# Kernel optimization log

Hardware: AMD Instinct MI355X
Metric: run time of the kernel (lower is better)

The kernel has to match this reference:

```python
import jax, jax.numpy as jnp
import numpy as np

NUM_HEADS = 8
DIM_HEAD = 64
GROUPS = 32
EPS = 1e-5


def setup_inputs() -> dict:
    key = jax.random.key(0)
    k1, k2, k3 = jax.random.split(key, 3)
    C = 512
    inner = NUM_HEADS * DIM_HEAD  # 512
    x = jax.random.normal(k1, (8, C, 32, 32), dtype=jnp.float32)
    gamma = jnp.ones((C,), dtype=jnp.float32)
    beta = jnp.zeros((C,), dtype=jnp.float32)
    w_qkv = jax.random.normal(k2, (3 * inner, C), dtype=jnp.float32) * 0.02
    w_out = jax.random.normal(k3, (C, inner), dtype=jnp.float32) * 0.02
    return {"x": x, "gamma": gamma, "beta": beta, "w_qkv": w_qkv, "w_out": w_out}


def group_norm(x, gamma, beta):
    b, c, h, w = x.shape
    xg = x.reshape(b, GROUPS, c // GROUPS, h, w)
    mean = jnp.mean(xg, axis=(2, 3, 4), keepdims=True)
    var = jnp.var(xg, axis=(2, 3, 4), keepdims=True)
    xn = ((xg - mean) * jax.lax.rsqrt(var + EPS)).reshape(b, c, h, w)
    return xn * gamma[None, :, None, None] + beta[None, :, None, None]


def reference(x, gamma, beta, w_qkv, w_out):
    b, c, h, w = x.shape
    H, d = NUM_HEADS, DIM_HEAD
    inner = H * d
    scale = d ** (-0.5)
    residual = x
    xn = group_norm(x, gamma, beta)
    # 1x1 conv (no bias) == channel matmul
    qkv = jnp.einsum('bchw,oc->bohw', xn, w_qkv)  # [b, 3*inner, h, w]
    q, k, v = jnp.split(qkv, 3, axis=1)
    def to_heads(t):
        # b (H d) h w -> b H (h w) d
        return t.reshape(b, H, d, h * w).transpose(0, 1, 3, 2)
    q, k, v = to_heads(q), to_heads(k), to_heads(v)
    attn = jnp.einsum('bhid,bhjd->bhij', q, k) * scale  # [b,H,hw,hw]
    attn = jax.nn.softmax(attn, axis=-1)
    out = jnp.einsum('bhij,bhjd->bhid', attn, v)  # [b,H,hw,d]
    # b H (h w) d -> b (H d) h w
    out = out.transpose(0, 1, 3, 2).reshape(b, inner, h, w)
    out = jnp.einsum('bchw,oc->bohw', out, w_out)
    return out + residual
```

## Files before the change

kernel.cpp:

```cpp
#include <hip/hip_runtime.h>


typedef __attribute__((ext_vector_type(8))) short bf16x8;
typedef __attribute__((ext_vector_type(4))) short bf16x4;
typedef __attribute__((ext_vector_type(4))) float f32x4;
typedef __attribute__((ext_vector_type(16))) float f32x16;

#define NB 8
#define NC 512
#define HW 1024
#define NHEAD 8
#define DHEAD 64
#define GROUPS 32
#define CPG 16
#define QKV_N 1536

#define GLL16(gaddr, ldsaddr)                                                  \
    __builtin_amdgcn_global_load_lds(                                          \
        (const __attribute__((address_space(1))) unsigned*)(gaddr),            \
        (__attribute__((address_space(3))) unsigned*)(ldsaddr), 16, 0, 0)

__device__ alignas(64) short g_xn[(size_t)8192 * 512];
__device__ alignas(64) short g_qkv[(size_t)8192 * 1536];
__device__ alignas(64) short g_vt[(size_t)64 * 64 * 1024];
__device__ alignas(64) short g_attno[(size_t)8192 * 512];
__device__ alignas(64) short g_wqkv[(size_t)1536 * 512];
__device__ alignas(64) short g_wout[(size_t)512 * 512];

__device__ __forceinline__ float b2f(short h) {
    union { unsigned u; float f; } v;
    v.u = ((unsigned)(unsigned short)h) << 16;
    return v.f;
}
__device__ __forceinline__ short f2b(float f) {
    union { float f; unsigned u; } v;
    v.f = f;
    unsigned r = v.u + 0x7fff + ((v.u >> 16) & 1);
    return (short)(r >> 16);
}

__global__ __launch_bounds__(256) void prep_kernel(
    const float* __restrict__ x, const float* __restrict__ gamma,
    const float* __restrict__ beta, const float* __restrict__ wqkv,
    const float* __restrict__ wout) {
    int tid = threadIdx.x;
    if (blockIdx.x >= 256) {
        int wb = blockIdx.x - 256;
        for (int i = wb * 256 + tid; i < 1536 * 512; i += 64 * 256) {
            float v = wqkv[i];
            if (i < 512 * 512) v *= 0.18033688011112042f;
            g_wqkv[i] = f2b(v);
        }
        for (int i = wb * 256 + tid; i < 512 * 512; i += 64 * 256)
            g_wout[i] = f2b(wout[i]);
        return;
    }
    int b = blockIdx.x >> 5, g = blockIdx.x & 31;
    __shared__ alignas(16) short tile[CPG][HW];
    __shared__ float red[2][4];
    __shared__ float sg[CPG], sb[CPG];
    if (tid < CPG) {
        int cg = g * CPG + tid;
        sg[tid] = gamma[cg];
        sb[tid] = beta[cg];
    }
    const float* xb = x + (size_t)b * NC * HW + (size_t)g * CPG * HW;
    float s1 = 0.f, s2 = 0.f;
    #pragma unroll
    for (int it = 0; it < 8; it++) {
        int idx = tid + it * 256;
        f32x4 v0 = *(const f32x4*)(xb + idx * 8);
        f32x4 v1 = *(const f32x4*)(xb + idx * 8 + 4);
        bf16x8 w;
        #pragma unroll
        for (int j = 0; j < 4; j++) {
            s1 += v0[j] + v1[j]; s2 += v0[j] * v0[j] + v1[j] * v1[j];
            w[j] = f2b(v0[j]); w[j + 4] = f2b(v1[j]);
        }
        *(bf16x8*)(&((short*)tile)[idx * 8]) = w;
    }
    #pragma unroll
    for (int off = 32; off; off >>= 1) { s1 += __shfl_xor(s1, off); s2 += __shfl_xor(s2, off); }
    int wid = tid >> 6;
    if ((tid & 63) == 0) { red[0][wid] = s1; red[1][wid] = s2; }
    __syncthreads();
    float t1 = red[0][0] + red[0][1] + red[0][2] + red[0][3];
    float t2 = red[1][0] + red[1][1] + red[1][2] + red[1][3];
    float mean = t1 * (1.f / 16384.f);
    float var  = t2 * (1.f / 16384.f) - mean * mean;
    float inv  = rsqrtf(var + 1e-5f);
    #pragma unroll
    for (int p = 0; p < 4; p++) {
        int s = tid * 4 + p;
        bf16x8 pk0, pk1;
        #pragma unroll
        for (int cc = 0; cc < 8; cc++) {
            pk0[cc] = f2b((b2f(tile[cc][s])     - mean) * inv * sg[cc]     + sb[cc]);
            pk1[cc] = f2b((b2f(tile[cc + 8][s]) - mean) * inv * sg[cc + 8] + sb[cc + 8]);
        }
        size_t dst = ((size_t)(b * HW + s)) * NC + g * CPG;
        *(bf16x8*)(g_xn + dst)     = pk0;
        *(bf16x8*)(g_xn + dst + 8) = pk1;
    }
}

__global__ __launch_bounds__(256) void gemm_qkv() {
    const int K = NC;
    int tid = threadIdx.x, lane = tid & 63, wid = tid >> 6;
    int quad = lane >> 4, l15 = lane & 15;
    int row0 = blockIdx.x * 128;
    int col0 = blockIdx.y * 128;
    __shared__ alignas(16) short sa[128 * 64];
    __shared__ alignas(16) short sbuf[128 * 64];
    int r_lo = lane >> 3;
    int s_log = (lane & 7) ^ r_lo;
    int swz = l15 & 7;
    const short* ga = g_xn   + (size_t)(row0 + wid * 32 + r_lo) * K + s_log * 8;
    const short* gb = g_wqkv + (size_t)(col0 + wid * 32 + r_lo) * K + s_log * 8;
    int mw = (wid >> 1) * 64, nw = (wid & 1) * 64;
    f32x4 acc[4][4] = {};
    for (int k = 0; k < K; k += 64) {
        #pragma unroll
        for (int c = 0; c < 4; c++) {
            GLL16(ga + (size_t)(c * 8) * K + k, &sa[(wid * 32 + c * 8) * 64]);
            GLL16(gb + (size_t)(c * 8) * K + k, &sbuf[(wid * 32 + c * 8) * 64]);
        }
        __syncthreads();
        bf16x8 af0[4], af1[4], bf0[4], bf1[4];
        #pragma unroll
        for (int m = 0; m < 4; m++) {
            int row = mw + m * 16 + l15;
            af0[m] = *(const bf16x8*)&sa[row * 64 + ((quad ^ swz) * 8)];
            af1[m] = *(const bf16x8*)&sa[row * 64 + (((4 + quad) ^ swz) * 8)];
        }
        #pragma unroll
        for (int n = 0; n < 4; n++) {
            int row = nw + n * 16 + l15;
            bf0[n] = *(const bf16x8*)&sbuf[row * 64 + ((quad ^ swz) * 8)];
            bf1[n] = *(const bf16x8*)&sbuf[row * 64 + (((4 + quad) ^ swz) * 8)];
        }
        #pragma unroll
        for (int m = 0; m < 4; m++)
            #pragma unroll
            for (int n = 0; n < 4; n++) {
                acc[m][n] = __builtin_amdgcn_mfma_f32_16x16x32_bf16(af0[m], bf0[n], acc[m][n], 0, 0, 0);
                acc[m][n] = __builtin_amdgcn_mfma_f32_16x16x32_bf16(af1[m], bf1[n], acc[m][n], 0, 0, 0);
            }
        __syncthreads();
    }
    #pragma unroll
    for (int m = 0; m < 4; m++)
        #pragma unroll
        for (int n = 0; n < 4; n++)
            #pragma unroll
            for (int r = 0; r < 4; r++) {
                int row = row0 + mw + m * 16 + quad * 4 + r;
                int col = col0 + nw + n * 16 + l15;
                g_qkv[(size_t)row * QKV_N + col] = f2b(acc[m][n][r]);
            }
}

__global__ __launch_bounds__(256) void transpose_v() {
    int bh = blockIdx.x & 63, st = blockIdx.x >> 6;
    int b = bh >> 3, h = bh & 7;
    int tid = threadIdx.x;
    __shared__ alignas(16) short tile[64][72];
    int s0 = st * 64;
    #pragma unroll
    for (int cc = 0; cc < 2; cc++) {
        int idx = tid + cc * 256;
        int s = idx >> 3, dc = idx & 7;
        *(bf16x8*)&tile[s][dc * 8] =
            *(const bf16x8*)(g_qkv + ((size_t)(b * HW + s0 + s)) * QKV_N + 1024 + h * DHEAD + dc * 8);
    }
    __syncthreads();
    #pragma unroll
    for (int cc = 0; cc < 2; cc++) {
        int idx = tid + cc * 256;
        int d = idx & 63, sc = idx >> 6;
        bf16x8 o;
        #pragma unroll
        for (int j = 0; j < 8; j++) o[j] = tile[sc * 8 + j][d];
        *(bf16x8*)(g_vt + ((size_t)(bh * 64 + d)) * HW + s0 + sc * 8) = o;
    }
}

__global__ __launch_bounds__(256) void attn_kernel() {
    int bh = blockIdx.x & 63, qt = blockIdx.x >> 6;
    int b = bh >> 3, h = bh & 7;
    int tid = threadIdx.x, lane = tid & 63, wid = tid >> 6;
    int l31 = lane & 31, hl = lane >> 5;
    __shared__ alignas(16) short kt[2][64 * 64];
    __shared__ alignas(16) short vt[2][64 * 64];
    int qrow0 = qt * 128 + wid * 32;

    const short* qb = g_qkv + ((size_t)(b * HW + qrow0 + l31)) * QKV_N + h * DHEAD + hl * 8;
    bf16x8 aq[4];
    #pragma unroll
    for (int ks = 0; ks < 4; ks++) aq[ks] = *(const bf16x8*)(qb + ks * 16);

    f32x16 acc_o0 = {}, acc_o1 = {}, acc_l = {};
    bf16x8 vone;
    #pragma unroll
    for (int j = 0; j < 8; j++) vone[j] = (short)0x3f80;

    int r_lo = lane >> 3;
    int s_log = (lane & 7) ^ r_lo;

    auto stage = [&](int it, int bufi) {
        int t0 = it * 64;
        #pragma unroll
        for (int c = 0; c < 2; c++) {
            int r = wid * 16 + c * 8 + r_lo;
            GLL16(g_qkv + ((size_t)(b * HW + t0 + r)) * QKV_N + 512 + h * DHEAD + s_log * 8,
                  &kt[bufi][(wid * 16 + c * 8) * 64]);
            GLL16(g_vt + ((size_t)(bh * 64 + r)) * HW + t0 + s_log * 8,
                  &vt[bufi][(wid * 16 + c * 8) * 64]);
        }
    };

    auto qk = [&](int buf, f32x16& z0, f32x16& z1) {
        #pragma unroll
        for (int ks = 0; ks < 4; ks++) {
            int g0 = ks * 2 + hl;
            int rowa = l31;
            bf16x8 k0 = *(const bf16x8*)&kt[buf][rowa * 64 + ((g0 ^ (rowa & 7)) * 8)];
            z0 = __builtin_amdgcn_mfma_f32_32x32x16_bf16(k0, aq[ks], z0, 0, 0, 0);
            int rowb = 32 + l31;
            bf16x8 k1 = *(const bf16x8*)&kt[buf][rowb * 64 + ((g0 ^ (rowb & 7)) * 8)];
            z1 = __builtin_amdgcn_mfma_f32_32x32x16_bf16(k1, aq[ks], z1, 0, 0, 0);
        }
    };

    auto exppack = [&](const f32x16& z0, const f32x16& z1, bf16x8* ap) {
        unsigned u0[8], u1[8];
        #pragma unroll
        for (int p = 0; p < 8; p++) {
            float e0, e1, e2, e3;
            asm("v_exp_f32 %0, %1" : "=v"(e0) : "v"(z0[2 * p]));
            asm("v_exp_f32 %0, %1" : "=v"(e1) : "v"(z0[2 * p + 1]));
            asm("v_exp_f32 %0, %1" : "=v"(e2) : "v"(z1[2 * p]));
            asm("v_exp_f32 %0, %1" : "=v"(e3) : "v"(z1[2 * p + 1]));
            asm("v_cvt_pk_bf16_f32 %0, %1, %2" : "=v"(u0[p]) : "v"(e0), "v"(e1));
            asm("v_cvt_pk_bf16_f32 %0, %1, %2" : "=v"(u1[p]) : "v"(e2), "v"(e3));
        }
        #pragma unroll
        for (int th = 0; th < 2; th++) {
            #pragma unroll
            for (int ks1 = 0; ks1 < 2; ks1++) {
                unsigned x0 = th ? u1[4 * ks1]     : u0[4 * ks1];
                unsigned y0 = th ? u1[4 * ks1 + 2] : u0[4 * ks1 + 2];
                unsigned x1 = th ? u1[4 * ks1 + 1] : u0[4 * ks1 + 1];
                unsigned y1 = th ? u1[4 * ks1 + 3] : u0[4 * ks1 + 3];
                asm("v_permlane32_swap_b32 %0, %1" : "+v"(x0), "+v"(y0));
                asm("v_permlane32_swap_b32 %0, %1" : "+v"(x1), "+v"(y1));
                union { unsigned w[4]; bf16x8 v; } pa;
                pa.w[0] = x0; pa.w[1] = x1; pa.w[2] = y0; pa.w[3] = y1;
                ap[th * 2 + ks1] = pa.v;
            }
        }
    };

    stage(0, 0);
    __syncthreads();
    stage(1, 1);
    bf16x8 ap_cur[4];
    {
        f32x16 z0 = {}, z1 = {};
        qk(0, z0, z1);
        exppack(z0, z1, ap_cur);
    }

    for (int it = 0; it < 15; it++) {
        int cur = it & 1, alt = cur ^ 1;
        bf16x8 bv0[4], bv1[4];
        #pragma unroll
        for (int ks = 0; ks < 4; ks++) {
            int gt = ks * 2 + hl;
            int rowd0 = l31;
            bv0[ks] = *(const bf16x8*)&vt[cur][rowd0 * 64 + ((gt ^ (rowd0 & 7)) * 8)];
            int rowd1 = 32 + l31;
            bv1[ks] = *(const bf16x8*)&vt[cur][rowd1 * 64 + ((gt ^ (rowd1 & 7)) * 8)];
        }
        __syncthreads();
        if (it < 14) stage(it + 2, cur);
        f32x16 z0 = {}, z1 = {};
        qk(alt, z0, z1);
        bf16x8 ap_next[4];
        exppack(z0, z1, ap_next);
        #pragma unroll
        for (int ks = 0; ks < 4; ks++)
            acc_l = __builtin_amdgcn_mfma_f32_32x32x16_bf16(ap_cur[ks], vone, acc_l, 0, 0, 0);
        #pragma unroll
        for (int ks = 0; ks < 4; ks++) {
            acc_o0 = __builtin_amdgcn_mfma_f32_32x32x16_bf16(ap_cur[ks], bv0[ks], acc_o0, 0, 0, 0);
            acc_o1 = __builtin_amdgcn_mfma_f32_32x32x16_bf16(ap_cur[ks], bv1[ks], acc_o1, 0, 0, 0);
        }
        #pragma unroll
        for (int ks = 0; ks < 4; ks++) ap_cur[ks] = ap_next[ks];
    }
    {
        #pragma unroll
        for (int ks = 0; ks < 4; ks++)
            acc_l = __builtin_amdgcn_mfma_f32_32x32x16_bf16(ap_cur[ks], vone, acc_l, 0, 0, 0);
        #pragma unroll
        for (int ks = 0; ks < 4; ks++) {
            int gt = ks * 2 + hl;
            int rowd0 = l31;
            bf16x8 bv0 = *(const bf16x8*)&vt[1][rowd0 * 64 + ((gt ^ (rowd0 & 7)) * 8)];
            acc_o0 = __builtin_amdgcn_mfma_f32_32x32x16_bf16(ap_cur[ks], bv0, acc_o0, 0, 0, 0);
            int rowd1 = 32 + l31;
            bf16x8 bv1 = *(const bf16x8*)&vt[1][rowd1 * 64 + ((gt ^ (rowd1 & 7)) * 8)];
            acc_o1 = __builtin_amdgcn_mfma_f32_32x32x16_bf16(ap_cur[ks], bv1, acc_o1, 0, 0, 0);
        }
    }
    #pragma unroll
    for (int r = 0; r < 16; r++) {
        int m = (r & 3) + 8 * (r >> 2) + 4 * hl;
        float invl = 1.f / acc_l[r];
        size_t row = (size_t)(b * HW + qrow0 + m);
        g_attno[row * NC + h * DHEAD + l31]      = f2b(acc_o0[r] * invl);
        g_attno[row * NC + h * DHEAD + 32 + l31] = f2b(acc_o1[r] * invl);
    }
}

__global__ __launch_bounds__(256) void gemm_out(
    const float* __restrict__ xres, float* __restrict__ out) {
    const int K = NC;
    int tid = threadIdx.x, lane = tid & 63, wid = tid >> 6;
    int quad = lane >> 4, l15 = lane & 15;
    int row0 = blockIdx.x * 128;
    int col0 = blockIdx.y * 128;
    __shared__ alignas(16) short sa[128 * 32];
    __shared__ alignas(16) short sbuf[128 * 32];
    int srow = wid * 32 + (lane >> 2);
    int scol = (lane & 3) * 8;
    const short* ga = g_wout  + (size_t)(row0 + srow) * K + scol;
    const short* gb = g_attno + (size_t)(col0 + srow) * K + scol;
    short* la = sa   + wid * 1024;
    short* lb = sbuf + wid * 1024;
    int mw = (wid >> 1) * 64, nw = (wid & 1) * 64;
    f32x4 acc[4][4] = {};
    for (int k = 0; k < K; k += 32) {
        GLL16(ga + k, la);
        GLL16(ga + (size_t)16 * K + k, la + 512);
        GLL16(gb + k, lb);
        GLL16(gb + (size_t)16 * K + k, lb + 512);
        __syncthreads();
        bf16x8 af[4], bfv[4];
        #pragma unroll
        for (int m = 0; m < 4; m++) af[m]  = *(const bf16x8*)&sa[(mw + m * 16 + l15) * 32 + quad * 8];
        #pragma unroll
        for (int n = 0; n < 4; n++) bfv[n] = *(const bf16x8*)&sbuf[(nw + n * 16 + l15) * 32 + quad * 8];
        #pragma unroll
        for (int m = 0; m < 4; m++)
            #pragma unroll
            for (int n = 0; n < 4; n++)
                acc[m][n] = __builtin_amdgcn_mfma_f32_16x16x32_bf16(af[m], bfv[n], acc[m][n], 0, 0, 0);
        __syncthreads();
    }
    #pragma unroll
    for (int m = 0; m < 4; m++)
        #pragma unroll
        for (int n = 0; n < 4; n++)
            #pragma unroll
            for (int r = 0; r < 4; r++) {
                int o  = row0 + mw + m * 16 + quad * 4 + r;
                int bs = col0 + nw + n * 16 + l15;
                size_t addr = (size_t)(bs >> 10) * ((size_t)NC * HW) + (size_t)o * HW + (bs & 1023);
                out[addr] = acc[m][n][r] + xres[addr];
            }
}

extern "C" void kernel_launch(void* const* d_in, const int* in_sizes, int n_in,
                              void* d_out, int out_size, void* d_ws, size_t ws_size,
                              hipStream_t stream) {
    const float* x     = (const float*)d_in[0];
    const float* gamma = (const float*)d_in[1];
    const float* beta  = (const float*)d_in[2];
    const float* wqkv  = (const float*)d_in[3];
    const float* wout  = (const float*)d_in[4];
    float* out = (float*)d_out;

    prep_kernel<<<dim3(320), dim3(256), 0, stream>>>(x, gamma, beta, wqkv, wout);
    gemm_qkv<<<dim3(64, 12), dim3(256), 0, stream>>>();
    transpose_v<<<dim3(1024), dim3(256), 0, stream>>>();
    attn_kernel<<<dim3(512), dim3(256), 0, stream>>>();
    gemm_out<<<dim3(4, 64), dim3(256), 0, stream>>>(x, out);
}
```

Baseline: 151.8 us.

## Triple-buffer QKV GEMM LDS tiles with prefetch two K-steps ahead

Restructures the QKV projection GEMM main loop to use three LDS buffers of 32-wide K tiles instead of one 64-wide tile. Global-to-LDS loads for tile t+2 are issued while tile t is consumed, with explicit vmcnt waits and barriers in place of full syncthreads, so load latency overlaps the MFMA work. The swizzle is adapted to the 32-column layout. The trade-off is twice as many loop iterations with extra barriers per step, and the hand-written waitcnt counts must match the number of loads in flight.

```diff
diff --git a/kernel.cpp b/kernel.cpp
--- a/kernel.cpp
+++ b/kernel.cpp
@@ -110,43 +110,53 @@
     int quad = lane >> 4, l15 = lane & 15;
     int row0 = blockIdx.x * 128;
     int col0 = blockIdx.y * 128;
-    __shared__ alignas(16) short sa[128 * 64];
-    __shared__ alignas(16) short sbuf[128 * 64];
-    int r_lo = lane >> 3;
-    int s_log = (lane & 7) ^ r_lo;
-    int swz = l15 & 7;
-    const short* ga = g_xn   + (size_t)(row0 + wid * 32 + r_lo) * K + s_log * 8;
-    const short* gb = g_wqkv + (size_t)(col0 + wid * 32 + r_lo) * K + s_log * 8;
+    __shared__ alignas(16) short sa[3][128 * 32];
+    __shared__ alignas(16) short sbuf[3][128 * 32];
+    int r_lo = lane >> 2;
+    int gsrc = lane & 3;
     int mw = (wid >> 1) * 64, nw = (wid & 1) * 64;
+
+    auto stageT = [&](int t, int slot) {
+        int k0 = t * 32;
+        #pragma unroll
+        for (int c = 0; c < 2; c++) {
+            int r = c * 64 + wid * 16 + r_lo;
+            int gl = (gsrc ^ ((r >> 1) & 3)) * 8;
+            GLL16(g_xn   + (size_t)(row0 + r) * K + k0 + gl,
+                  &sa[slot][(c * 64 + wid * 16) * 32]);
+            GLL16(g_wqkv + (size_t)(col0 + r) * K + k0 + gl,
+                  &sbuf[slot][(c * 64 + wid * 16) * 32]);
+        }
+    };
+
     f32x4 acc[4][4] = {};
-    for (int k = 0; k < K; k += 64) {
-        #pragma unroll
-        for (int c = 0; c < 4; c++) {
-            GLL16(ga + (size_t)(c * 8) * K + k, &sa[(wid * 32 + c * 8) * 64]);
-            GLL16(gb + (size_t)(c * 8) * K + k, &sbuf[(wid * 32 + c * 8) * 64]);
-        }
-        __syncthreads();
-        bf16x8 af0[4], af1[4], bf0[4], bf1[4];
+    stageT(0, 0);
+    stageT(1, 1);
+    for (int t = 0; t < 16; t++) {
+        int slot = t % 3;
+        if (t < 15) { asm volatile("s_waitcnt vmcnt(4)" ::: "memory"); }
+        else        { asm volatile("s_waitcnt vmcnt(0)" ::: "memory"); }
+        __builtin_amdgcn_s_barrier();
+        if (t + 2 < 16) stageT(t + 2, (t + 2) % 3);
+        bf16x8 af[4], bfv[4];
         #pragma unroll
         for (int m = 0; m < 4; m++) {
             int row = mw + m * 16 + l15;
-            af0[m] = *(const bf16x8*)&sa[row * 64 + ((quad ^ swz) * 8)];
-            af1[m] = *(const bf16x8*)&sa[row * 64 + (((4 + quad) ^ swz) * 8)];
+            af[m] = *(const bf16x8*)&sa[slot][row * 32 + ((quad ^ ((row >> 1) & 3)) * 8)];
         }
         #pragma unroll
         for (int n = 0; n < 4; n++) {
             int row = nw + n * 16 + l15;
-            bf0[n] = *(const bf16x8*)&sbuf[row * 64 + ((quad ^ swz) * 8)];
-            bf1[n] = *(const bf16x8*)&sbuf[row * 64 + (((4 + quad) ^ swz) * 8)];
-        }
+            bfv[n] = *(const bf16x8*)&sbuf[slot][row * 32 + ((quad ^ ((row >> 1) & 3)) * 8)];
+        }
+        asm volatile("s_waitcnt lgkmcnt(0)" ::: "memory");
+        __builtin_amdgcn_sched_barrier(0);
+        __builtin_amdgcn_s_barrier();
         #pragma unroll
         for (int m = 0; m < 4; m++)
             #pragma unroll
-            for (int n = 0; n < 4; n++) {
-                acc[m][n] = __builtin_amdgcn_mfma_f32_16x16x32_bf16(af0[m], bf0[n], acc[m][n], 0, 0, 0);
-                acc[m][n] = __builtin_amdgcn_mfma_f32_16x16x32_bf16(af1[m], bf1[n], acc[m][n], 0, 0, 0);
-            }
-        __syncthreads();
+            for (int n = 0; n < 4; n++)
+                acc[m][n] = __builtin_amdgcn_mfma_f32_16x16x32_bf16(af[m], bfv[n], acc[m][n], 0, 0, 0);
     }
     #pragma unroll
     for (int m = 0; m < 4; m++)
```

Measured after the change: 154.4 us. About the same (+1.7%).
